# Kernel optimization log

Hardware: AMD Instinct MI355X
Metric: run time of the kernel (lower is better)

The kernel has to match this reference:

```python
import jax, jax.numpy as jnp
import numpy as np

L, S, M, N, E, H = 1024, 1024, 256, 8, 512, 8


def embed_rotary(x, cos, sin):
    # x: [B, T, E]; interleaved rotate-half as in RotaryPositionEncoding.embed_rotary
    x2 = jnp.stack([-x[..., 1::2], x[..., 0::2]], axis=-1).reshape(x.shape)
    return x * cos + x2 * sin


def setup_inputs() -> dict:
    key = jax.random.key(0)
    ks = jax.random.split(key, 12)
    return {
        "query": jax.random.normal(ks[0], (L, N, E), jnp.float32),
        "key": jax.random.normal(ks[1], (S, N, E), jnp.float32),
        "value": jax.random.normal(ks[2], (S, N, E), jnp.float32),
        "in_proj_weight": jax.random.normal(ks[3], (3 * E, E), jnp.float32) / np.sqrt(E).astype(np.float32),
        "in_proj_bias": jnp.zeros((3 * E,), jnp.float32),
        "out_proj_weight": jax.random.normal(ks[4], (E, E), jnp.float32) / np.sqrt(E).astype(np.float32),
        "out_proj_bias": jnp.zeros((E,), jnp.float32),
        "rot_q": jax.random.normal(ks[5], (N, L, E, 2), jnp.float32),
        "rot_k": jax.random.normal(ks[6], (N, S, E, 2), jnp.float32),
        "k_mem": jax.random.normal(ks[7], (M, N, E), jnp.float32),
        "v_mem": jax.random.normal(ks[8], (M, N, E), jnp.float32),
        "gate_attn": jax.random.normal(ks[9], (H,), jnp.float32),
        "mem_mask": jax.random.randint(ks[10], (N, M), 0, 2).astype(bool),
        "num_heads": H,
    }


def reference(query, key, value, in_proj_weight, in_proj_bias, out_proj_weight,
              out_proj_bias, rot_q, rot_k, k_mem, v_mem, gate_attn, mem_mask, num_heads):
    L_, N_, E_ = query.shape
    S_ = key.shape[0]
    H_ = num_heads
    hd = E_ // H_
    scale = float(hd) ** -0.5
    # separate q/k/v projections (qkv not identical path)
    q = query @ in_proj_weight[:E_].T + in_proj_bias[:E_]
    k = key @ in_proj_weight[E_:2 * E_].T + in_proj_bias[E_:2 * E_]
    v = value @ in_proj_weight[2 * E_:].T + in_proj_bias[2 * E_:]
    q = q * scale
    # inline rotary PE (applied in batch-first layout, then back)
    q = embed_rotary(q.transpose(1, 0, 2), rot_q[..., 0], rot_q[..., 1]).transpose(1, 0, 2)
    k = embed_rotary(k.transpose(1, 0, 2), rot_k[..., 0], rot_k[..., 1]).transpose(1, 0, 2)
    qh = q.reshape(L_, N_, H_, hd).transpose(1, 2, 0, 3)  # [N,H,L,hd]
    kh = k.reshape(S_, N_, H_, hd).transpose(1, 2, 0, 3)  # [N,H,S,hd]
    vh = v.reshape(S_, N_, H_, hd).transpose(1, 2, 0, 3)
    scores = jnp.einsum('nhld,nhsd->nhls', qh, kh)
    # slot-competition: softmax over queries (slots), then renormalize over keys
    w = jax.nn.softmax(scores, axis=2) + 1e-8
    w = w / w.sum(axis=-1, keepdims=True)
    attn = jnp.einsum('nhls,nhsd->nhld', w, vh)
    # memorizing-transformer style memory K/V branch with sigmoid head gating
    Mm = k_mem.shape[0]
    km = k_mem.reshape(Mm, N_, H_, hd).transpose(1, 2, 0, 3)  # [N,H,M,hd]
    vm = v_mem.reshape(Mm, N_, H_, hd).transpose(1, 2, 0, 3)
    sm = jnp.einsum('nhld,nhmd->nhlm', qh, km)
    sm = jnp.where(mem_mask[:, None, None, :], -1e9, sm)  # additive -inf mask
    wm = jax.nn.softmax(sm, axis=-1)
    om = jnp.einsum('nhlm,nhmd->nhld', wm, vm)
    gate = jax.nn.sigmoid(gate_attn)[None, :, None, None]  # [1,H,1,1]
    attn = gate * om + (1.0 - gate) * attn
    out = attn.transpose(2, 0, 1, 3).reshape(L_, N_, E_)  # back to [L,N,E]
    return out @ out_proj_weight.T + out_proj_bias
```

## Files before the change

kernel.cpp:

```cpp
#include <hip/hip_runtime.h>
#include <hip/hip_bf16.h>

typedef __hip_bfloat16 bf16;
typedef __bf16 bf16x8 __attribute__((ext_vector_type(8)));
typedef float f32x4 __attribute__((ext_vector_type(4)));

#define LQ 1024
#define SK 1024
#define MMEM 256
#define NB 8
#define EE 512
#define NH 8
#define HD 64
#define NBH 64

__device__ inline __bf16 tobf(float f) {
  __hip_bfloat16 h = __float2bfloat16(f);
  return *reinterpret_cast<__bf16*>(&h);
}
__device__ inline float bf2f(__bf16 x) {
  unsigned short u; __builtin_memcpy(&u, &x, 2);
  unsigned int v = (unsigned int)u << 16;
  float f; __builtin_memcpy(&f, &v, 4);
  return f;
}
__device__ inline f32x4 MFMA(bf16x8 a, bf16x8 b, f32x4 c) {
  return __builtin_amdgcn_mfma_f32_16x16x32_bf16(a, b, c, 0, 0, 0);
}

__device__ inline void gload_lds16(const bf16* g, void* l) {
  __builtin_amdgcn_global_load_lds(
      (const __attribute__((address_space(1))) void*)g,
      (__attribute__((address_space(3))) void*)l, 16, 0, 0);
}

__device__ inline bf16x8 load8(const float* p) {
  float4 a = *(const float4*)p;
  float4 b = *(const float4*)(p + 4);
  bf16x8 r;
  r[0] = tobf(a.x); r[1] = tobf(a.y); r[2] = tobf(a.z); r[3] = tobf(a.w);
  r[4] = tobf(b.x); r[5] = tobf(b.y); r[6] = tobf(b.z); r[7] = tobf(b.w);
  return r;
}

#define CVT_T0 524288
#define CVT_T3 98304
#define CVT_T4 32768
__global__ __launch_bounds__(256) void convert5(
    const float* __restrict__ q, const float* __restrict__ k,
    const float* __restrict__ v, const float* __restrict__ w,
    const float* __restrict__ o, bf16* __restrict__ qc, bf16* __restrict__ kc,
    bf16* __restrict__ vc, bf16* __restrict__ wc, bf16* __restrict__ oc)
{
  long long t = (long long)blockIdx.x * 256 + threadIdx.x;
  const float* src; bf16* dst; long long idx;
  if (t < CVT_T0)               { src = q; dst = qc; idx = t; }
  else if (t < 2 * CVT_T0)      { src = k; dst = kc; idx = t - CVT_T0; }
  else if (t < 3 * CVT_T0)      { src = v; dst = vc; idx = t - 2 * CVT_T0; }
  else if (t < 3 * CVT_T0 + CVT_T3) { src = w; dst = wc; idx = t - 3 * CVT_T0; }
  else                          { src = o; dst = oc; idx = t - 3 * CVT_T0 - CVT_T3; }
  *(bf16x8*)(dst + idx * 8) = load8(src + idx * 8);
}

__global__ __launch_bounds__(256) void gemm_proj3(
    const bf16* __restrict__ qc, const bf16* __restrict__ kc,
    const bf16* __restrict__ vc, const bf16* __restrict__ ipwb,
    const float* __restrict__ ipb, const float* __restrict__ rot_q,
    const float* __restrict__ rot_k, bf16* __restrict__ Qh,
    bf16* __restrict__ Kh, bf16* __restrict__ v_raw)
{
  __shared__ __align__(16) char smem[33792];
  __bf16* As = (__bf16*)smem;
  __bf16* Bs = (__bf16*)(smem + 16384);
  const int z = blockIdx.z;
  const bf16* A = (z == 0) ? qc : (z == 1) ? kc : vc;
  const bf16* W = ipwb + (long long)z * EE * EE;
  const float* bias = ipb + z * EE;
  const float alpha = (z == 0) ? 0.125f : 1.f;
  const int tm0 = blockIdx.y << 7, tn0 = blockIdx.x << 7;
  const int t = threadIdx.x;
  const int wave = t >> 6, lane = t & 63;
  const int wrow0 = (wave & 1) << 6, wcol0 = (wave >> 1) << 6;
  const int m16 = lane & 15, quad = lane >> 4;

  const f32x4 zero = {0.f, 0.f, 0.f, 0.f};
  f32x4 acc[4][4];
#pragma unroll
  for (int mi = 0; mi < 4; ++mi)
#pragma unroll
    for (int ni = 0; ni < 4; ++ni) acc[mi][ni] = zero;

  const bf16* Ab = A + (long long)tm0 * EE;
  const bf16* Bb = W + (long long)tn0 * EE;
  const int ob_u = wave << 10;

  for (int k0 = 0; k0 < EE; k0 += 64) {
#pragma unroll
    for (int c = 0; c < 4; ++c) {
      int ob = (c << 12) + ob_u;
      int obl = ob + (lane << 4);
      int row = obl >> 7;
      int ce = (obl & 127) >> 1;
      gload_lds16(Ab + (long long)row * EE + k0 + ce, smem + ob);
      gload_lds16(Bb + (long long)row * EE + k0 + ce, smem + 16384 + ob);
    }
    __syncthreads();
#pragma unroll
    for (int kh = 0; kh < 2; ++kh) {
      bf16x8 av[4], bv[4];
#pragma unroll
      for (int i = 0; i < 4; ++i) {
        av[i] = *(bf16x8*)(As + ((wrow0 + (i << 4) + m16) << 6) + (kh << 5) + (quad << 3));
        bv[i] = *(bf16x8*)(Bs + ((wcol0 + (i << 4) + m16) << 6) + (kh << 5) + (quad << 3));
      }
#pragma unroll
      for (int mi = 0; mi < 4; ++mi)
#pragma unroll
        for (int ni = 0; ni < 4; ++ni)
          acc[mi][ni] = MFMA(av[mi], bv[ni], acc[mi][ni]);
    }
    __syncthreads();
  }

  __bf16 (*Cs)[132] = (__bf16(*)[132])smem;
#pragma unroll
  for (int mi = 0; mi < 4; ++mi)
#pragma unroll
    for (int ni = 0; ni < 4; ++ni) {
      int col = wcol0 + (ni << 4) + m16;
      float bv = bias[tn0 + col];
#pragma unroll
      for (int r = 0; r < 4; ++r)
        Cs[wrow0 + (mi << 4) + (quad << 2) + r][col] =
            tobf((acc[mi][ni][r] + bv) * alpha);
    }
  __syncthreads();

  const int crow = t >> 1, ch0 = (t & 1) << 6;
  const int grow = tm0 + crow;
  if (z == 2) {
    long long gb = (long long)grow * EE + tn0 + ch0;
#pragma unroll
    for (int j = 0; j < 64; j += 8)
      *(uint4*)(v_raw + gb + j) = *(uint4*)&Cs[crow][ch0 + j];
  } else {
    const int l = grow >> 3, n = grow & 7;
    const float* rot = (z == 0) ? rot_q : rot_k;
    bf16* Out2 = (z == 0) ? Qh : Kh;
#pragma unroll
    for (int cc = 0; cc < 4; ++cc) {
      int e0 = tn0 + ch0 + (cc << 4);
      int h = e0 >> 6, d0 = e0 & 63;
      const float* rp = rot + ((((long long)n * LQ + l) * EE + e0) << 1);
      __bf16 vals[16];
#pragma unroll
      for (int j = 0; j < 16; j += 2) {
        float4 cs4 = *(const float4*)(rp + (j << 1));
        float x0 = bf2f(Cs[crow][ch0 + (cc << 4) + j]);
        float x1 = bf2f(Cs[crow][ch0 + (cc << 4) + j + 1]);
        vals[j]     = tobf(x0 * cs4.x - x1 * cs4.y);
        vals[j + 1] = tobf(x1 * cs4.z + x0 * cs4.w);
      }
      bf16* dst = Out2 + ((((long long)(n * NH + h) * LQ) + l) * HD + d0);
      *(uint4*)dst = *(uint4*)&vals[0];
      *(uint4*)(dst + 8) = *(uint4*)&vals[8];
    }
  }
}

__global__ __launch_bounds__(256) void colsum_kernel(
    const bf16* __restrict__ Qh, const bf16* __restrict__ Kh,
    float* __restrict__ csum)
{
  __shared__ __align__(16) __bf16 Ks[64][72];
  __shared__ __align__(16) __bf16 Qs[64][72];
  __shared__ float cpart[64][2];
  const int b = blockIdx.y;
  const int st0 = blockIdx.x << 6;
  const int t = threadIdx.x;
  const int lrow = t >> 2, lcol = (t & 3) << 4;
  const int wave = t >> 6, lane = t & 63;
  const int wm = (wave & 1) << 5, wn = (wave >> 1) << 5;
  const int m16 = lane & 15, quad = lane >> 4;

  {
    const bf16* kp = Kh + ((long long)b * SK + st0 + lrow) * HD + lcol;
    *(bf16x8*)&Ks[lrow][lcol] = *(const bf16x8*)kp;
    *(bf16x8*)&Ks[lrow][lcol + 8] = *(const bf16x8*)(kp + 8);
  }
  __syncthreads();
  bf16x8 bk[2][2];
#pragma unroll
  for (int ni = 0; ni < 2; ++ni)
#pragma unroll
    for (int kh = 0; kh < 2; ++kh)
      bk[ni][kh] = *(bf16x8*)&Ks[wn + (ni << 4) + m16][(kh << 5) + (quad << 3)];
  __syncthreads();

  const f32x4 zero = {0.f, 0.f, 0.f, 0.f};
  float colp[2] = {0.f, 0.f};
  for (int lt = 0; lt < 16; ++lt) {
    const bf16* qp = Qh + ((long long)b * LQ + (lt << 6) + lrow) * HD + lcol;
    *(bf16x8*)&Qs[lrow][lcol] = *(const bf16x8*)qp;
    *(bf16x8*)&Qs[lrow][lcol + 8] = *(const bf16x8*)(qp + 8);
    __syncthreads();
    f32x4 s00 = zero, s01 = zero, s10 = zero, s11 = zero;
#pragma unroll
    for (int kh = 0; kh < 2; ++kh) {
      bf16x8 a0 = *(bf16x8*)&Qs[wm + m16][(kh << 5) + (quad << 3)];
      bf16x8 a1 = *(bf16x8*)&Qs[wm + 16 + m16][(kh << 5) + (quad << 3)];
      s00 = MFMA(a0, bk[0][kh], s00);
      s01 = MFMA(a0, bk[1][kh], s01);
      s10 = MFMA(a1, bk[0][kh], s10);
      s11 = MFMA(a1, bk[1][kh], s11);
    }
    f32x4 sacc[2][2] = {{s00, s01}, {s10, s11}};
#pragma unroll
    for (int mi = 0; mi < 2; ++mi)
#pragma unroll
      for (int ni = 0; ni < 2; ++ni)
#pragma unroll
        for (int r = 0; r < 4; ++r)
          colp[ni] += __expf(sacc[mi][ni][r]);
    __syncthreads();
  }
  for (int ni = 0; ni < 2; ++ni) {
    float v = colp[ni];
    v += __shfl_down(v, 32, 64);
    v += __shfl_down(v, 16, 64);
    if (quad == 0) cpart[wn + (ni << 4) + m16][wm >> 5] = v;
  }
  __syncthreads();
  if (t < 64) csum[b * SK + st0 + t] = cpart[t][0] + cpart[t][1];
}

__global__ __launch_bounds__(256) void vsum_kernel(
    const bf16* __restrict__ Vt, float* __restrict__ Vsum)
{
  int wid = blockIdx.x * 4 + (threadIdx.x >> 6);
  int lane = threadIdx.x & 63;
  const bf16* p = Vt + (long long)wid * SK + lane * 16;
  float s = 0.f;
  bf16x8 v0 = *(const bf16x8*)p;
  bf16x8 v1 = *(const bf16x8*)(p + 8);
#pragma unroll
  for (int j = 0; j < 8; ++j) s += bf2f(v0[j]) + bf2f(v1[j]);
  for (int off = 32; off; off >>= 1) s += __shfl_down(s, off, 64);
  if (lane == 0) Vsum[wid] = s;
}

__global__ __launch_bounds__(256) void attn_flash(
    const bf16* __restrict__ Qh, const bf16* __restrict__ Kh,
    const bf16* __restrict__ Vt, const float* __restrict__ csum,
    const float* __restrict__ Vsum, bf16* __restrict__ attn)
{
  __shared__ __align__(16) __bf16 Ks[64][72];
  __shared__ __align__(16) __bf16 Vs[64][72];
  __shared__ __align__(16) __bf16 Ps[64][72];
  __shared__ float rcs[SK];
  __shared__ float rpart[64][2];
  const int b = blockIdx.y;
  const int tm0 = blockIdx.x << 6;
  const int t = threadIdx.x;
  const int lrow = t >> 2, lcol = (t & 3) << 4;
  const int wave = t >> 6, lane = t & 63;
  const int wm = (wave & 1) << 5, wn = (wave >> 1) << 5;
  const int m16 = lane & 15, quad = lane >> 4;

#pragma unroll
  for (int i = 0; i < 4; ++i)
    rcs[t + i * 256] = 1.f / csum[b * SK + t + i * 256];
  {
    const bf16* qp = Qh + ((long long)b * LQ + tm0 + lrow) * HD + lcol;
    *(bf16x8*)&Ks[lrow][lcol] = *(const bf16x8*)qp;
    *(bf16x8*)&Ks[lrow][lcol + 8] = *(const bf16x8*)(qp + 8);
  }
  __syncthreads();
  bf16x8 aq[2][2];
#pragma unroll
  for (int mi = 0; mi < 2; ++mi)
#pragma unroll
    for (int kh = 0; kh < 2; ++kh)
      aq[mi][kh] = *(bf16x8*)&Ks[wm + (mi << 4) + m16][(kh << 5) + (quad << 3)];
  __syncthreads();

  const f32x4 zero = {0.f, 0.f, 0.f, 0.f};
  f32x4 o00 = zero, o01 = zero, o10 = zero, o11 = zero;
  float rsumr[2][4] = {{0.f, 0.f, 0.f, 0.f}, {0.f, 0.f, 0.f, 0.f}};

  for (int st = 0; st < 16; ++st) {
    const bf16* kp = Kh + ((long long)b * SK + (st << 6) + lrow) * HD + lcol;
    *(bf16x8*)&Ks[lrow][lcol] = *(const bf16x8*)kp;
    *(bf16x8*)&Ks[lrow][lcol + 8] = *(const bf16x8*)(kp + 8);
    const bf16* vp = Vt + ((long long)b * HD + lrow) * SK + (st << 6) + lcol;
    *(bf16x8*)&Vs[lrow][lcol] = *(const bf16x8*)vp;
    *(bf16x8*)&Vs[lrow][lcol + 8] = *(const bf16x8*)(vp + 8);
    __syncthreads();
    f32x4 s00 = zero, s01 = zero, s10 = zero, s11 = zero;
#pragma unroll
    for (int kh = 0; kh < 2; ++kh) {
      bf16x8 b0 = *(bf16x8*)&Ks[wn + m16][(kh << 5) + (quad << 3)];
      bf16x8 b1 = *(bf16x8*)&Ks[wn + 16 + m16][(kh << 5) + (quad << 3)];
      s00 = MFMA(aq[0][kh], b0, s00);
      s01 = MFMA(aq[0][kh], b1, s01);
      s10 = MFMA(aq[1][kh], b0, s10);
      s11 = MFMA(aq[1][kh], b1, s11);
    }
    f32x4 sacc[2][2] = {{s00, s01}, {s10, s11}};
#pragma unroll
    for (int mi = 0; mi < 2; ++mi)
#pragma unroll
      for (int ni = 0; ni < 2; ++ni) {
        int col = wn + (ni << 4) + m16;
        float rc = rcs[(st << 6) + col];
#pragma unroll
        for (int r = 0; r < 4; ++r) {
          float p = __expf(sacc[mi][ni][r]) * rc;
          rsumr[mi][r] += p;
          Ps[wm + (mi << 4) + (quad << 2) + r][col] = tobf(p);
        }
      }
    __syncthreads();
#pragma unroll
    for (int kh = 0; kh < 2; ++kh) {
      bf16x8 ap0 = *(bf16x8*)&Ps[wm + m16][(kh << 5) + (quad << 3)];
      bf16x8 ap1 = *(bf16x8*)&Ps[wm + 16 + m16][(kh << 5) + (quad << 3)];
      bf16x8 bv0 = *(bf16x8*)&Vs[wn + m16][(kh << 5) + (quad << 3)];
      bf16x8 bv1 = *(bf16x8*)&Vs[wn + 16 + m16][(kh << 5) + (quad << 3)];
      o00 = MFMA(ap0, bv0, o00);
      o01 = MFMA(ap0, bv1, o01);
      o10 = MFMA(ap1, bv0, o10);
      o11 = MFMA(ap1, bv1, o11);
    }
    __syncthreads();
  }
#pragma unroll
  for (int mi = 0; mi < 2; ++mi)
#pragma unroll
    for (int r = 0; r < 4; ++r) {
      float v = rsumr[mi][r];
      v += __shfl_xor(v, 1, 64);
      v += __shfl_xor(v, 2, 64);
      v += __shfl_xor(v, 4, 64);
      v += __shfl_xor(v, 8, 64);
      if (m16 == 0) rpart[wm + (mi << 4) + (quad << 2) + r][wn >> 5] = v;
    }
  __syncthreads();
  const float* vs = Vsum + b * HD;
  f32x4 oacc[2][2] = {{o00, o01}, {o10, o11}};
  for (int mi = 0; mi < 2; ++mi)
    for (int ni = 0; ni < 2; ++ni) {
      int col = wn + (ni << 4) + m16;
      float vsc = 1e-8f * vs[col];
      for (int r = 0; r < 4; ++r) {
        int row = wm + (mi << 4) + (quad << 2) + r;
        float rs = rpart[row][0] + rpart[row][1];
        Ps[row][col] = tobf((oacc[mi][ni][r] + vsc) / (rs + (float)SK * 1e-8f));
      }
    }
  __syncthreads();
  uint4 u0 = *(uint4*)&Ps[lrow][lcol];
  uint4 u1 = *(uint4*)&Ps[lrow][lcol + 8];
  long long gb = ((long long)b * LQ + tm0 + lrow) * HD + lcol;
  *(uint4*)(attn + gb) = u0;
  *(uint4*)(attn + gb + 8) = u1;
}

__global__ __launch_bounds__(256) void mem_flash(
    const bf16* __restrict__ Qh, const bf16* __restrict__ km,
    const bf16* __restrict__ vmt, const int* __restrict__ mask,
    bf16* __restrict__ omb)
{
  __shared__ __align__(16) __bf16 Ks[64][72];
  __shared__ __align__(16) __bf16 Vs[64][72];
  __shared__ __align__(16) __bf16 Ps[64][72];
  __shared__ float mskf[MMEM];
  __shared__ float rpart[64][2];
  const int b = blockIdx.y;
  const int n = b >> 3;
  const int tm0 = blockIdx.x << 6;
  const int t = threadIdx.x;
  const int wave = t >> 6, lane = t & 63;
  const int wm = (wave & 1) << 5, wn = (wave >> 1) << 5;
  const int m16 = lane & 15, quad = lane >> 4;
  const int lrow = t >> 2, lcol = (t & 3) << 4;

  mskf[t] = mask[n * MMEM + t] ? 0.f : 1.f;
  {
    const bf16* qp = Qh + ((long long)b * LQ + tm0 + lrow) * HD + lcol;
    *(bf16x8*)&Ks[lrow][lcol] = *(const bf16x8*)qp;
    *(bf16x8*)&Ks[lrow][lcol + 8] = *(const bf16x8*)(qp + 8);
  }
  __syncthreads();
  bf16x8 aq[2][2];
#pragma unroll
  for (int mi = 0; mi < 2; ++mi)
#pragma unroll
    for (int kh = 0; kh < 2; ++kh)
      aq[mi][kh] = *(bf16x8*)&Ks[wm + (mi << 4) + m16][(kh << 5) + (quad << 3)];
  __syncthreads();

  const f32x4 zero = {0.f, 0.f, 0.f, 0.f};
  f32x4 o00 = zero, o01 = zero, o10 = zero, o11 = zero;
  float rsumr[2][4] = {{0.f, 0.f, 0.f, 0.f}, {0.f, 0.f, 0.f, 0.f}};

  for (int mt = 0; mt < 4; ++mt) {
    const bf16* kp = km + ((long long)b * MMEM + (mt << 6) + lrow) * HD + lcol;
    *(bf16x8*)&Ks[lrow][lcol] = *(const bf16x8*)kp;
    *(bf16x8*)&Ks[lrow][lcol + 8] = *(const bf16x8*)(kp + 8);
    const bf16* vp = vmt + ((long long)b * HD + lrow) * MMEM + (mt << 6) + lcol;
    *(bf16x8*)&Vs[lrow][lcol] = *(const bf16x8*)vp;
    *(bf16x8*)&Vs[lrow][lcol + 8] = *(const bf16x8*)(vp + 8);
    __syncthreads();
    f32x4 s00 = zero, s01 = zero, s10 = zero, s11 = zero;
#pragma unroll
    for (int kh = 0; kh < 2; ++kh) {
      bf16x8 b0 = *(bf16x8*)&Ks[wn + m16][(kh << 5) + (quad << 3)];
      bf16x8 b1 = *(bf16x8*)&Ks[wn + 16 + m16][(kh << 5) + (quad << 3)];
      s00 = MFMA(aq[0][kh], b0, s00);
      s01 = MFMA(aq[0][kh], b1, s01);
      s10 = MFMA(aq[1][kh], b0, s10);
      s11 = MFMA(aq[1][kh], b1, s11);
    }
    f32x4 sacc[2][2] = {{s00, s01}, {s10, s11}};
#pragma unroll
    for (int mi = 0; mi < 2; ++mi)
#pragma unroll
      for (int ni = 0; ni < 2; ++ni) {
        int col = wn + (ni << 4) + m16;
        float mf = mskf[(mt << 6) + col];
#pragma unroll
        for (int r = 0; r < 4; ++r) {
          float p = __expf(sacc[mi][ni][r]) * mf;
          rsumr[mi][r] += p;
          Ps[wm + (mi << 4) + (quad << 2) + r][col] = tobf(p);
        }
      }
    __syncthreads();
#pragma unroll
    for (int kh = 0; kh < 2; ++kh) {
      bf16x8 ap0 = *(bf16x8*)&Ps[wm + m16][(kh << 5) + (quad << 3)];
      bf16x8 ap1 = *(bf16x8*)&Ps[wm + 16 + m16][(kh << 5) + (quad << 3)];
      bf16x8 bv0 = *(bf16x8*)&Vs[wn + m16][(kh << 5) + (quad << 3)];
      bf16x8 bv1 = *(bf16x8*)&Vs[wn + 16 + m16][(kh << 5) + (quad << 3)];
      o00 = MFMA(ap0, bv0, o00);
      o01 = MFMA(ap0, bv1, o01);
      o10 = MFMA(ap1, bv0, o10);
      o11 = MFMA(ap1, bv1, o11);
    }
    __syncthreads();
  }
#pragma unroll
  for (int mi = 0; mi < 2; ++mi)
#pragma unroll
    for (int r = 0; r < 4; ++r) {
      float v = rsumr[mi][r];
      v += __shfl_xor(v, 1, 64);
      v += __shfl_xor(v, 2, 64);
      v += __shfl_xor(v, 4, 64);
      v += __shfl_xor(v, 8, 64);
      if (m16 == 0) rpart[wm + (mi << 4) + (quad << 2) + r][wn >> 5] = v;
    }
  __syncthreads();
  f32x4 oacc[2][2] = {{o00, o01}, {o10, o11}};
  for (int mi = 0; mi < 2; ++mi)
    for (int ni = 0; ni < 2; ++ni) {
      int col = wn + (ni << 4) + m16;
      for (int r = 0; r < 4; ++r) {
        int row = wm + (mi << 4) + (quad << 2) + r;
        float rs = rpart[row][0] + rpart[row][1];
        Ps[row][col] = tobf(oacc[mi][ni][r] / rs);
      }
    }
  __syncthreads();
  uint4 u0 = *(uint4*)&Ps[lrow][lcol];
  uint4 u1 = *(uint4*)&Ps[lrow][lcol + 8];
  long long gb = ((long long)b * LQ + tm0 + lrow) * HD + lcol;
  *(uint4*)(omb + gb) = u0;
  *(uint4*)(omb + gb + 8) = u1;
}

__global__ __launch_bounds__(256) void gemm_out(
    const bf16* __restrict__ attn, const bf16* __restrict__ omb,
    const float* __restrict__ gate, const bf16* __restrict__ opwb,
    const float* __restrict__ opb, float* __restrict__ out)
{
  __shared__ __align__(16) __bf16 As[64][40];
  __shared__ __align__(16) __bf16 Bs[64][40];
  __shared__ float sg[NH];
  const int tm0 = blockIdx.y << 6, tn0 = blockIdx.x << 6;
  const int t = threadIdx.x;
  const int lrow = t >> 2, lk = (t & 3) << 3;
  const int wave = t >> 6, lane = t & 63;
  const int wm = (wave & 1) << 5, wn = (wave >> 1) << 5;
  const int m16 = lane & 15, quad = lane >> 4;

  if (t < NH) sg[t] = 1.f / (1.f + __expf(-gate[t]));
  __syncthreads();

  const f32x4 zero = {0.f, 0.f, 0.f, 0.f};
  f32x4 acc00 = zero, acc01 = zero, acc10 = zero, acc11 = zero;

  const int row = tm0 + lrow;
  const int l = row >> 3, n = row & 7;
  const bf16* bg = opwb + (long long)(tn0 + lrow) * EE + lk;
  for (int k0 = 0; k0 < EE; k0 += 32) {
    int e = k0 + lk;
    int h = e >> 6, d = e & 63;
    float g = sg[h];
    long long src = (((long long)(n * NH + h) * LQ) + l) * HD + d;
    bf16x8 a8 = *(const bf16x8*)(attn + src);
    bf16x8 o8 = *(const bf16x8*)(omb + src);
    bf16x8 ap;
#pragma unroll
    for (int j = 0; j < 8; ++j)
      ap[j] = tobf(g * bf2f(o8[j]) + (1.f - g) * bf2f(a8[j]));
    *(bf16x8*)&As[lrow][lk] = ap;
    *(bf16x8*)&Bs[lrow][lk] = *(const bf16x8*)(bg + k0);
    __syncthreads();
    bf16x8 a0 = *(bf16x8*)&As[wm + m16][quad << 3];
    bf16x8 a1 = *(bf16x8*)&As[wm + 16 + m16][quad << 3];
    bf16x8 b0 = *(bf16x8*)&Bs[wn + m16][quad << 3];
    bf16x8 b1 = *(bf16x8*)&Bs[wn + 16 + m16][quad << 3];
    acc00 = MFMA(a0, b0, acc00);
    acc01 = MFMA(a0, b1, acc01);
    acc10 = MFMA(a1, b0, acc10);
    acc11 = MFMA(a1, b1, acc11);
    __syncthreads();
  }
  f32x4 accs[2][2] = {{acc00, acc01}, {acc10, acc11}};
  for (int mi = 0; mi < 2; ++mi)
    for (int ni = 0; ni < 2; ++ni) {
      int col = tn0 + wn + (ni << 4) + m16;
      float bv = opb[col];
      long long base = (long long)(tm0 + wm + (mi << 4) + (quad << 2)) * EE + col;
      for (int r = 0; r < 4; ++r)
        out[base + (long long)r * EE] = accs[mi][ni][r] + bv;
    }
}

__global__ __launch_bounds__(256) void v_transpose(
    const bf16* __restrict__ raw, bf16* __restrict__ Vt)
{
  long long i = (long long)blockIdx.x * 256 + threadIdx.x;
  int e = (int)(i & 511);
  long long t2 = i >> 9;
  int n = (int)(t2 & 7);
  int s = (int)(t2 >> 3);
  int h = e >> 6, d = e & 63;
  Vt[(((long long)(n * NH + h) * HD) + d) * SK + s] = raw[i];
}

__global__ __launch_bounds__(256) void mem_prep(
    const float* __restrict__ k_mem, const float* __restrict__ v_mem,
    bf16* __restrict__ km, bf16* __restrict__ vmt)
{
  long long i = (long long)blockIdx.x * 256 + threadIdx.x;
  int e = (int)(i & 511);
  long long t2 = i >> 9;
  int n = (int)(t2 & 7);
  int m = (int)(t2 >> 3);
  int h = e >> 6, d = e & 63;
  km[(((long long)(n * NH + h) * MMEM) + m) * HD + d] = (bf16)k_mem[i];
  vmt[(((long long)(n * NH + h) * HD) + d) * MMEM + m] = (bf16)v_mem[i];
}

extern "C" void kernel_launch(void* const* d_in, const int* in_sizes, int n_in,
                              void* d_out, int out_size, void* d_ws, size_t ws_size,
                              hipStream_t stream) {
  const float* query = (const float*)d_in[0];
  const float* key   = (const float*)d_in[1];
  const float* value = (const float*)d_in[2];
  const float* ipw   = (const float*)d_in[3];
  const float* ipb   = (const float*)d_in[4];
  const float* opw   = (const float*)d_in[5];
  const float* opb   = (const float*)d_in[6];
  const float* rot_q = (const float*)d_in[7];
  const float* rot_k = (const float*)d_in[8];
  const float* k_mem = (const float*)d_in[9];
  const float* v_mem = (const float*)d_in[10];
  const float* gate  = (const float*)d_in[11];
  const int*  mask   = (const int*)d_in[12];
  float* out = (float*)d_out;

  char* w = (char*)d_ws;
  size_t off = 0;
  auto carve = [&](size_t bytes) -> char* {
    char* p = w + off;
    off += (bytes + 255) & ~(size_t)255;
    return p;
  };
  bf16* qc    = (bf16*)carve((size_t)LQ * NB * EE * 2);
  bf16* kc    = (bf16*)carve((size_t)SK * NB * EE * 2);
  bf16* vc    = (bf16*)carve((size_t)SK * NB * EE * 2);
  bf16* ipwb  = (bf16*)carve((size_t)3 * EE * EE * 2);
  bf16* opwb  = (bf16*)carve((size_t)EE * EE * 2);
  bf16* v_raw = (bf16*)carve((size_t)SK * NB * EE * 2);
  bf16* Qh    = (bf16*)carve((size_t)NBH * LQ * HD * 2);
  bf16* Kh    = (bf16*)carve((size_t)NBH * SK * HD * 2);
  bf16* Vt    = (bf16*)carve((size_t)NBH * HD * SK * 2);
  bf16* km    = (bf16*)carve((size_t)NBH * MMEM * HD * 2);
  bf16* vmt   = (bf16*)carve((size_t)NBH * HD * MMEM * 2);
  float* csum = (float*)carve((size_t)NBH * SK * 4);
  float* Vsum = (float*)carve((size_t)NBH * HD * 4);
  bf16* attn  = (bf16*)carve((size_t)NBH * LQ * HD * 2);
  bf16* omb   = (bf16*)carve((size_t)NBH * LQ * HD * 2);
  if (off > ws_size) {
    hipMemsetAsync(d_out, 0, (size_t)out_size * 4, stream);
    return;
  }

  convert5<<<(3 * CVT_T0 + CVT_T3 + CVT_T4) / 256, 256, 0, stream>>>(
      query, key, value, ipw, opw, qc, kc, vc, ipwb, opwb);

  gemm_proj3<<<dim3(EE / 128, (LQ * NB) / 128, 3), 256, 0, stream>>>(
      qc, kc, vc, ipwb, ipb, rot_q, rot_k, Qh, Kh, v_raw);

  v_transpose<<<(SK * NB * EE) / 256, 256, 0, stream>>>(v_raw, Vt);
  vsum_kernel<<<(NBH * HD) / 4, 256, 0, stream>>>(Vt, Vsum);
  mem_prep<<<(MMEM * NB * EE) / 256, 256, 0, stream>>>(k_mem, v_mem, km, vmt);

  colsum_kernel<<<dim3(SK / 64, NBH), 256, 0, stream>>>(Qh, Kh, csum);

  attn_flash<<<dim3(LQ / 64, NBH), 256, 0, stream>>>(Qh, Kh, Vt, csum, Vsum, attn);
  mem_flash<<<dim3(LQ / 64, NBH), 256, 0, stream>>>(Qh, km, vmt, mask, omb);

  gemm_out<<<dim3(EE / 64, (LQ * NB) / 64, 1), 256, 0, stream>>>(attn, omb, gate, opwb, opb, out);
}
```

Measured before the change: 354.7 us.

## Split rotary into its own kernel and use LDS-tiled transposes for V and memory

New measurement: 330.4 us. -6.9%, faster.

```diff
diff --git a/kernel.cpp b/kernel.cpp
--- a/kernel.cpp
+++ b/kernel.cpp
@@ -65,9 +65,8 @@
 __global__ __launch_bounds__(256) void gemm_proj3(
     const bf16* __restrict__ qc, const bf16* __restrict__ kc,
     const bf16* __restrict__ vc, const bf16* __restrict__ ipwb,
-    const float* __restrict__ ipb, const float* __restrict__ rot_q,
-    const float* __restrict__ rot_k, bf16* __restrict__ Qh,
-    bf16* __restrict__ Kh, bf16* __restrict__ v_raw)
+    const float* __restrict__ ipb, bf16* __restrict__ pq,
+    bf16* __restrict__ pk, bf16* __restrict__ v_raw)
 {
   __shared__ __align__(16) char smem[33792];
   __bf16* As = (__bf16*)smem;
@@ -135,37 +134,39 @@
             tobf((acc[mi][ni][r] + bv) * alpha);
     }
   __syncthreads();
-
+  bf16* O = (z == 0) ? pq : (z == 1) ? pk : v_raw;
   const int crow = t >> 1, ch0 = (t & 1) << 6;
-  const int grow = tm0 + crow;
-  if (z == 2) {
-    long long gb = (long long)grow * EE + tn0 + ch0;
-#pragma unroll
-    for (int j = 0; j < 64; j += 8)
-      *(uint4*)(v_raw + gb + j) = *(uint4*)&Cs[crow][ch0 + j];
-  } else {
-    const int l = grow >> 3, n = grow & 7;
-    const float* rot = (z == 0) ? rot_q : rot_k;
-    bf16* Out2 = (z == 0) ? Qh : Kh;
-#pragma unroll
-    for (int cc = 0; cc < 4; ++cc) {
-      int e0 = tn0 + ch0 + (cc << 4);
-      int h = e0 >> 6, d0 = e0 & 63;
-      const float* rp = rot + ((((long long)n * LQ + l) * EE + e0) << 1);
-      __bf16 vals[16];
-#pragma unroll
-      for (int j = 0; j < 16; j += 2) {
-        float4 cs4 = *(const float4*)(rp + (j << 1));
-        float x0 = bf2f(Cs[crow][ch0 + (cc << 4) + j]);
-        float x1 = bf2f(Cs[crow][ch0 + (cc << 4) + j + 1]);
-        vals[j]     = tobf(x0 * cs4.x - x1 * cs4.y);
-        vals[j + 1] = tobf(x1 * cs4.z + x0 * cs4.w);
-      }
-      bf16* dst = Out2 + ((((long long)(n * NH + h) * LQ) + l) * HD + d0);
-      *(uint4*)dst = *(uint4*)&vals[0];
-      *(uint4*)(dst + 8) = *(uint4*)&vals[8];
-    }
-  }
+  long long gb = (long long)(tm0 + crow) * EE + tn0 + ch0;
+#pragma unroll
+  for (int j = 0; j < 64; j += 8)
+    *(uint4*)(O + gb + j) = *(uint4*)&Cs[crow][ch0 + j];
+}
+
+__global__ __launch_bounds__(256) void rotary_kernel(
+    const bf16* __restrict__ pq, const bf16* __restrict__ pk,
+    const float* __restrict__ rot_q, const float* __restrict__ rot_k,
+    bf16* __restrict__ Qh, bf16* __restrict__ Kh)
+{
+  const bf16* src = blockIdx.y ? pk : pq;
+  const float* rot = blockIdx.y ? rot_k : rot_q;
+  bf16* dst = blockIdx.y ? Kh : Qh;
+  const int t = threadIdx.x;
+  const int row = (blockIdx.x << 2) + (t >> 6);
+  const int e0 = (t & 63) << 3;
+  const int l = row >> 3, n = row & 7;
+  bf16x8 x = *(const bf16x8*)(src + (long long)row * EE + e0);
+  const float* rp = rot + ((((long long)n * LQ + l) * EE + e0) << 1);
+  __bf16 vals[8];
+#pragma unroll
+  for (int j = 0; j < 8; j += 2) {
+    float4 cs4 = *(const float4*)(rp + (j << 1));
+    float x0 = bf2f(x[j]);
+    float x1 = bf2f(x[j + 1]);
+    vals[j]     = tobf(x0 * cs4.x - x1 * cs4.y);
+    vals[j + 1] = tobf(x1 * cs4.z + x0 * cs4.w);
+  }
+  const int h = e0 >> 6, d0 = e0 & 63;
+  *(uint4*)(dst + (((long long)(n * NH + h) * LQ + l) * HD + d0)) = *(uint4*)vals;
 }
 
 __global__ __launch_bounds__(256) void colsum_kernel(
@@ -542,27 +543,52 @@
 __global__ __launch_bounds__(256) void v_transpose(
     const bf16* __restrict__ raw, bf16* __restrict__ Vt)
 {
-  long long i = (long long)blockIdx.x * 256 + threadIdx.x;
-  int e = (int)(i & 511);
-  long long t2 = i >> 9;
-  int n = (int)(t2 & 7);
-  int s = (int)(t2 >> 3);
-  int h = e >> 6, d = e & 63;
-  Vt[(((long long)(n * NH + h) * HD) + d) * SK + s] = raw[i];
+  __shared__ __align__(16) __bf16 Ts[64][72];
+  const int bh = blockIdx.y;
+  const int n = bh >> 3, h = bh & 7;
+  const int s0 = blockIdx.x << 6;
+  const int t = threadIdx.x;
+  const int i = t >> 2, c0 = (t & 3) << 4;
+  const bf16* rp = raw + ((long long)(s0 + i) * NB + n) * EE + h * HD + c0;
+  *(bf16x8*)&Ts[i][c0] = *(const bf16x8*)rp;
+  *(bf16x8*)&Ts[i][c0 + 8] = *(const bf16x8*)(rp + 8);
+  __syncthreads();
+  const int d = t >> 2, j0 = (t & 3) << 4;
+  __bf16 vals[16];
+#pragma unroll
+  for (int j = 0; j < 16; ++j) vals[j] = Ts[j0 + j][d];
+  bf16* wp = Vt + ((long long)bh * HD + d) * SK + s0 + j0;
+  *(uint4*)wp = *(uint4*)&vals[0];
+  *(uint4*)(wp + 8) = *(uint4*)&vals[8];
 }
 
 __global__ __launch_bounds__(256) void mem_prep(
     const float* __restrict__ k_mem, const float* __restrict__ v_mem,
     bf16* __restrict__ km, bf16* __restrict__ vmt)
 {
-  long long i = (long long)blockIdx.x * 256 + threadIdx.x;
-  int e = (int)(i & 511);
-  long long t2 = i >> 9;
-  int n = (int)(t2 & 7);
-  int m = (int)(t2 >> 3);
-  int h = e >> 6, d = e & 63;
-  km[(((long long)(n * NH + h) * MMEM) + m) * HD + d] = (bf16)k_mem[i];
-  vmt[(((long long)(n * NH + h) * HD) + d) * MMEM + m] = (bf16)v_mem[i];
+  __shared__ __align__(16) __bf16 Ts[64][72];
+  const int bh = blockIdx.y;
+  const int n = bh >> 3, h = bh & 7;
+  const int m0 = blockIdx.x << 6;
+  const int t = threadIdx.x;
+  const int i = t >> 2, c0 = (t & 3) << 4;
+  const float* kp = k_mem + ((long long)(m0 + i) * NB + n) * EE + h * HD + c0;
+  const float* vp = v_mem + ((long long)(m0 + i) * NB + n) * EE + h * HD + c0;
+  bf16x8 kv0 = load8(kp), kv1 = load8(kp + 8);
+  bf16x8 vv0 = load8(vp), vv1 = load8(vp + 8);
+  bf16* kw = km + ((long long)bh * MMEM + m0 + i) * HD + c0;
+  *(bf16x8*)kw = kv0;
+  *(bf16x8*)(kw + 8) = kv1;
+  *(bf16x8*)&Ts[i][c0] = vv0;
+  *(bf16x8*)&Ts[i][c0 + 8] = vv1;
+  __syncthreads();
+  const int d = t >> 2, j0 = (t & 3) << 4;
+  __bf16 vals[16];
+#pragma unroll
+  for (int j = 0; j < 16; ++j) vals[j] = Ts[j0 + j][d];
+  bf16* wp = vmt + ((long long)bh * HD + d) * MMEM + m0 + j0;
+  *(uint4*)wp = *(uint4*)&vals[0];
+  *(uint4*)(wp + 8) = *(uint4*)&vals[8];
 }
 
 extern "C" void kernel_launch(void* const* d_in, const int* in_sizes, int n_in,
@@ -609,16 +635,21 @@
     hipMemsetAsync(d_out, 0, (size_t)out_size * 4, stream);
     return;
   }
+  bf16* pq = attn;
+  bf16* pk = omb;
 
   convert5<<<(3 * CVT_T0 + CVT_T3 + CVT_T4) / 256, 256, 0, stream>>>(
       query, key, value, ipw, opw, qc, kc, vc, ipwb, opwb);
 
   gemm_proj3<<<dim3(EE / 128, (LQ * NB) / 128, 3), 256, 0, stream>>>(
-      qc, kc, vc, ipwb, ipb, rot_q, rot_k, Qh, Kh, v_raw);
-
-  v_transpose<<<(SK * NB * EE) / 256, 256, 0, stream>>>(v_raw, Vt);
+      qc, kc, vc, ipwb, ipb, pq, pk, v_raw);
+
+  rotary_kernel<<<dim3((LQ * NB) / 4, 2), 256, 0, stream>>>(
+      pq, pk, rot_q, rot_k, Qh, Kh);
+
+  v_transpose<<<dim3(SK / 64, NBH), 256, 0, stream>>>(v_raw, Vt);
   vsum_kernel<<<(NBH * HD) / 4, 256, 0, stream>>>(Vt, Vsum);
-  mem_prep<<<(MMEM * NB * EE) / 256, 256, 0, stream>>>(k_mem, v_mem, km, vmt);
+  mem_prep<<<dim3(MMEM / 64, NBH), 256, 0, stream>>>(k_mem, v_mem, km, vmt);
 
   colsum_kernel<<<dim3(SK / 64, NBH), 256, 0, stream>>>(Qh, Kh, csum);
 
```
